# Optimization experiments

Measured on AMD Instinct MI355X. Metric: run time of the kernel, lower is better.

## Reference

```python
import jax, jax.numpy as jnp
import numpy as np


def setup_inputs() -> dict:
    key = jax.random.key(0)
    k1, k2, k3 = jax.random.split(key, 3)
    B, Cin, H, W = 32, 128, 56, 56
    E, Cout = 8, 128
    x = jax.random.normal(k1, (B, Cin, H, W), dtype=jnp.float32)
    conv_w = jax.random.normal(k2, (E, Cout, Cin, 3, 3), dtype=jnp.float32) * 0.05
    gate_w = jax.random.normal(k3, (E, Cin), dtype=jnp.float32) * 0.05
    gate_b = jnp.zeros((E,), dtype=jnp.float32)
    return {"x": x, "conv_w": conv_w, "gate_w": gate_w, "gate_b": gate_b, "top_k": 2}


def reference(x, conv_w, gate_w, gate_b, top_k):
    # x: [B, Cin, H, W]; conv_w: [E, Cout, Cin, 3, 3]
    E, Cout, Cin, kh, kw = conv_w.shape
    B = x.shape[0]
    # Gate: global average pool -> linear logits over experts
    gap = x.mean(axis=(2, 3))                      # [B, Cin]
    logits = gap @ gate_w.T + gate_b               # [B, E]
    vals, idx = jax.lax.top_k(logits, top_k)       # [B, k]
    w = jax.nn.softmax(vals, axis=-1)              # renormalize over selected experts
    weights = jnp.zeros((B, E), dtype=x.dtype).at[jnp.arange(B)[:, None], idx].set(w)
    # All experts via a single conv with stacked output channels (stride=1, pad=1 == SAME)
    y = jax.lax.conv_general_dilated(
        x, conv_w.reshape(E * Cout, Cin, kh, kw),
        window_strides=(1, 1), padding='SAME',
        dimension_numbers=('NCHW', 'OIHW', 'NCHW'))  # [B, E*Cout, H, W]
    y = y.reshape(B, E, Cout, y.shape[2], y.shape[3])
    out = jnp.einsum('be,bechw->bchw', weights, y)  # sparse-weight combine
    return out, weights
```

## Files before the change

### kernel.cpp

```cpp
#include <hip/hip_runtime.h>
#include <hip/hip_bf16.h>

constexpr int Bn   = 32;
constexpr int CIN  = 128;
constexpr int Hh   = 56;
constexpr int Ww   = 56;
constexpr int HW   = Hh * Ww;
constexpr int COUT = 128;
constexpr int En   = 8;

typedef __attribute__((ext_vector_type(8))) short bf16x8;
typedef __attribute__((ext_vector_type(4))) float f32x4;

struct GateInfo { int e0, e1; float w0, w1; };

constexpr size_t XB_OFF  = 0;
constexpr size_t XB_SZ   = (size_t)Bn * HW * CIN * 2;
constexpr size_t WW_OFF  = XB_OFF + XB_SZ;
constexpr size_t WW_SZ   = (size_t)Bn * 9 * COUT * CIN * 2;
constexpr size_t HS_OFF  = WW_OFF + WW_SZ;
constexpr size_t HS_SZ   = (size_t)Bn * Hh * CIN * 4;
constexpr size_t GAP_OFF = HS_OFF + HS_SZ;
constexpr size_t GAP_SZ  = (size_t)Bn * CIN * 4;
constexpr size_t GI_OFF  = GAP_OFF + GAP_SZ;

__global__ __launch_bounds__(256) void convert_kernel(const float* __restrict__ x,
        __hip_bfloat16* __restrict__ xbf, float* __restrict__ hsum) {
    __shared__ float lt[CIN * 57];
    int gid = blockIdx.x;
    int b = gid / Hh, h = gid % Hh;
    const float* xp = x + (size_t)b * CIN * HW + h * Ww;
    for (int u = threadIdx.x; u < CIN * Ww; u += 256) {
        int c = u / Ww, w = u % Ww;
        lt[c * 57 + w] = xp[(size_t)c * HW + w];
    }
    __syncthreads();
    __hip_bfloat16* xo = xbf + ((size_t)b * HW + h * Ww) * CIN;
    for (int u = threadIdx.x; u < CIN * Ww; u += 256) {
        int w = u >> 7, c = u & 127;
        xo[u] = __float2bfloat16(lt[c * 57 + w]);
    }
    if (threadIdx.x < CIN) {
        int c = threadIdx.x;
        float s = 0.f;
        #pragma unroll 8
        for (int w = 0; w < Ww; w++) s += lt[c * 57 + w];
        hsum[((size_t)b * Hh + h) * CIN + c] = s;
    }
}

__global__ void gap2_kernel(const float* __restrict__ hsum, float* __restrict__ gap) {
    int t = blockIdx.x * 256 + threadIdx.x;
    int b = t >> 7, c = t & 127;
    float s = 0.f;
    for (int h = 0; h < Hh; h++) s += hsum[((size_t)b * Hh + h) * CIN + c];
    gap[t] = s * (1.f / (float)HW);
}

__global__ void gate_kernel(const float* __restrict__ gap,
                            const float* __restrict__ gate_w,
                            const float* __restrict__ gate_b,
                            float* __restrict__ wout,
                            GateInfo* __restrict__ info) {
    __shared__ float logits[Bn][En];
    __shared__ GateInfo gi[Bn];
    int tid = threadIdx.x;
    int b = tid >> 3, e = tid & 7;
    float s = gate_b[e];
    const float* g = gap + b * CIN;
    const float* w = gate_w + e * CIN;
    #pragma unroll 8
    for (int c = 0; c < CIN; c++) s += g[c] * w[c];
    logits[b][e] = s;
    __syncthreads();
    if (tid < Bn) {
        float v[En];
        #pragma unroll
        for (int k = 0; k < En; k++) v[k] = logits[tid][k];
        int i0 = 0; float m0 = v[0];
        #pragma unroll
        for (int k = 1; k < En; k++) if (v[k] > m0) { m0 = v[k]; i0 = k; }
        int i1 = -1; float m1 = -1e30f;
        #pragma unroll
        for (int k = 0; k < En; k++) if (k != i0 && v[k] > m1) { m1 = v[k]; i1 = k; }
        float ex = expf(m1 - m0);
        float den = 1.f + ex;
        GateInfo t; t.e0 = i0; t.e1 = i1; t.w0 = 1.f / den; t.w1 = ex / den;
        gi[tid] = t;
        info[tid] = t;
    }
    __syncthreads();
    {
        int bb = tid >> 3, ee = tid & 7;
        GateInfo t = gi[bb];
        wout[tid] = (ee == t.e0) ? t.w0 : (ee == t.e1) ? t.w1 : 0.f;
    }
}

__global__ __launch_bounds__(256) void wcomb_kernel(const float* __restrict__ cw,
        const GateInfo* __restrict__ info, __hip_bfloat16* __restrict__ wws) {
    __shared__ __hip_bfloat16 wl[16 * 1152];
    int b = blockIdx.x >> 3, cg = blockIdx.x & 7;
    GateInfo gi = info[b];
    const float* p0 = cw + (size_t)gi.e0 * COUT * CIN * 9 + (size_t)cg * 16 * 1152;
    const float* p1 = cw + (size_t)gi.e1 * COUT * CIN * 9 + (size_t)cg * 16 * 1152;
    for (int u = threadIdx.x; u < 16 * 1152; u += 256)
        wl[u] = __float2bfloat16(gi.w0 * p0[u] + gi.w1 * p1[u]);
    __syncthreads();
    __hip_bfloat16* wo = wws + (size_t)b * 9 * COUT * CIN + (size_t)cg * 16 * CIN;
    for (int u = threadIdx.x; u < 16 * 1152; u += 256) {
        int t = u / 2048, rem = u & 2047;
        int co = rem >> 7, cin = rem & 127;
        wo[(size_t)t * COUT * CIN + co * CIN + cin] = wl[co * 1152 + cin * 9 + t];
    }
}

constexpr int US = 349;

__global__ __launch_bounds__(256, 2) void conv_mfma(
        const __hip_bfloat16* __restrict__ xbf,
        const __hip_bfloat16* __restrict__ wws,
        float* __restrict__ out) {
    __shared__ char xs[4 * US * 16];

    int gid = blockIdx.x;
    int b = gid / 28, rem = gid % 28;
    int cb = rem / 14, rb = rem % 14;
    int row0 = rb * 4, cout0 = cb * 64;
    int tid = threadIdx.x, wave = tid >> 6, lane = tid & 63;
    int wm = wave >> 1, wn = wave & 1;
    int l15 = lane & 15, lk = lane >> 4;

    int bbase[7];
    #pragma unroll
    for (int i = 0; i < 7; i++) {
        int p = wn * 112 + i * 16 + l15;
        int r = p / 56, c = p % 56;
        bbase[i] = (lk * US + (r * 58 + c)) * 16;
    }

    const __hip_bfloat16* wwb = wws + (size_t)b * 9 * COUT * CIN;
    int arow = cout0 + wm * 32 + l15;

    f32x4 acc[2][7];
    #pragma unroll
    for (int mt = 0; mt < 2; mt++)
        #pragma unroll
        for (int i = 0; i < 7; i++) acc[mt][i] = (f32x4){0.f, 0.f, 0.f, 0.f};

    for (int c0 = 0; c0 < CIN; c0 += 32) {
        __syncthreads();
        const __hip_bfloat16* xbb = xbf + (size_t)b * HW * CIN + c0;
        for (int u = tid; u < 1392; u += 256) {
            int rc = u >> 2, ul = u & 3;
            int lr = rc / 58, lc = rc % 58;
            int grow = row0 - 1 + lr, gw = lc - 1;
            int4 v = {0, 0, 0, 0};
            if ((unsigned)grow < 56u && (unsigned)gw < 56u)
                v = *(const int4*)(xbb + ((size_t)grow * 56 + gw) * CIN + ul * 8);
            *(int4*)(xs + (ul * US + rc) * 16) = v;
        }
        __syncthreads();

        const __hip_bfloat16* ap = wwb + (size_t)arow * CIN + c0 + lk * 8;
        #pragma unroll
        for (int t = 0; t < 9; t++) {
            const int dr = t / 3, dc = t % 3;
            bf16x8 a0 = *(const bf16x8*)(ap + (size_t)t * COUT * CIN);
            bf16x8 a1 = *(const bf16x8*)(ap + (size_t)t * COUT * CIN + 16 * CIN);
            const int toff = (dr * 58 + dc) * 16;
            #pragma unroll
            for (int i = 0; i < 7; i++) {
                bf16x8 bv = *(const bf16x8*)(xs + bbase[i] + toff);
                acc[0][i] = __builtin_amdgcn_mfma_f32_16x16x32_bf16(a0, bv, acc[0][i], 0, 0, 0);
                acc[1][i] = __builtin_amdgcn_mfma_f32_16x16x32_bf16(a1, bv, acc[1][i], 0, 0, 0);
            }
        }
    }

    float* outb = out + (size_t)b * COUT * HW + row0 * 56;
    #pragma unroll
    for (int mt = 0; mt < 2; mt++) {
        int cbase = cout0 + wm * 32 + mt * 16 + lk * 4;
        #pragma unroll
        for (int i = 0; i < 7; i++) {
            int pp = wn * 112 + i * 16 + l15;
            #pragma unroll
            for (int j = 0; j < 4; j++)
                outb[(size_t)(cbase + j) * HW + pp] = acc[mt][i][j];
        }
    }
}

extern "C" void kernel_launch(void* const* d_in, const int* in_sizes, int n_in,
                              void* d_out, int out_size, void* d_ws, size_t ws_size,
                              hipStream_t stream) {
    const float* x  = (const float*)d_in[0];
    const float* cw = (const float*)d_in[1];
    const float* gw = (const float*)d_in[2];
    const float* gb = (const float*)d_in[3];

    float* out = (float*)d_out;
    char* ws = (char*)d_ws;
    __hip_bfloat16* xbf  = (__hip_bfloat16*)(ws + XB_OFF);
    __hip_bfloat16* wws  = (__hip_bfloat16*)(ws + WW_OFF);
    float* hsum          = (float*)(ws + HS_OFF);
    float* gap           = (float*)(ws + GAP_OFF);
    GateInfo* info       = (GateInfo*)(ws + GI_OFF);
    float* wout = out + (size_t)Bn * COUT * HW;

    convert_kernel<<<Bn * Hh, 256, 0, stream>>>(x, xbf, hsum);
    gap2_kernel   <<<16,      256, 0, stream>>>(hsum, gap);
    gate_kernel   <<<1,       256, 0, stream>>>(gap, gw, gb, wout, info);
    wcomb_kernel  <<<Bn * 8,  256, 0, stream>>>(cw, info, wws);
    conv_mfma     <<<Bn * 2 * 14, 256, 0, stream>>>(xbf, wws, out);
}
```

Measured before the change: 182.0 us.

## Enlarge conv tile to 8 rows, map batches to XCDs, vectorize bf16 convert stores

The conv kernel now computes 8 output rows by 64 output channels per block. Each wave owns 112 pixels and all 64 channels, holding 4x7 accumulators, so every B-operand LDS read feeds four MFMAs instead of two. The grid drops to 448 blocks, and block indices are remapped so that blocks of the same batch land on the same XCD, which should improve L2 reuse of activations and weights. The convert kernel now packs 8 bf16 values into one 16-byte store instead of writing scalar bf16. The costs are higher register pressure (launch bounds now ask for 3 blocks per CU), a larger LDS tile, and fewer blocks, so the grid may fill the GPU less well.

After: 188.6 us. +3.6%, slower.

```diff
diff --git a/kernel.cpp b/kernel.cpp
--- a/kernel.cpp
+++ b/kernel.cpp
@@ -36,9 +36,15 @@
     }
     __syncthreads();
     __hip_bfloat16* xo = xbf + ((size_t)b * HW + h * Ww) * CIN;
-    for (int u = threadIdx.x; u < CIN * Ww; u += 256) {
-        int w = u >> 7, c = u & 127;
-        xo[u] = __float2bfloat16(lt[c * 57 + w]);
+    for (int u = threadIdx.x; u < 16 * Ww; u += 256) {
+        int w = u >> 4, cg = u & 15;
+        bf16x8 pk;
+        #pragma unroll
+        for (int j = 0; j < 8; j++) {
+            __hip_bfloat16 t = __float2bfloat16(lt[(cg * 8 + j) * 57 + w]);
+            pk[j] = *reinterpret_cast<short*>(&t);
+        }
+        *(bf16x8*)(xo + (size_t)w * CIN + cg * 8) = pk;
     }
     if (threadIdx.x < CIN) {
         int c = threadIdx.x;
@@ -115,20 +121,22 @@
     }
 }
 
-constexpr int US = 349;
-
-__global__ __launch_bounds__(256, 2) void conv_mfma(
+constexpr int USz = 581;
+
+__global__ __launch_bounds__(256, 3) void conv_mfma(
         const __hip_bfloat16* __restrict__ xbf,
         const __hip_bfloat16* __restrict__ wws,
         float* __restrict__ out) {
-    __shared__ char xs[4 * US * 16];
-
-    int gid = blockIdx.x;
-    int b = gid / 28, rem = gid % 28;
-    int cb = rem / 14, rb = rem % 14;
-    int row0 = rb * 4, cout0 = cb * 64;
+    __shared__ char xs[4 * USz * 16];
+
+    int bid = blockIdx.x;
+    int xcd = bid & 7, k = bid >> 3;
+    int b   = xcd * 4 + k / 14;
+    int rem = k % 14;
+    int cb  = rem / 7, rb = rem % 7;
+    int row0 = rb * 8, cout0 = cb * 64;
     int tid = threadIdx.x, wave = tid >> 6, lane = tid & 63;
-    int wm = wave >> 1, wn = wave & 1;
+    int wn = wave;
     int l15 = lane & 15, lk = lane >> 4;
 
     int bbase[7];
@@ -136,52 +144,55 @@
     for (int i = 0; i < 7; i++) {
         int p = wn * 112 + i * 16 + l15;
         int r = p / 56, c = p % 56;
-        bbase[i] = (lk * US + (r * 58 + c)) * 16;
+        bbase[i] = (lk * USz + (r * 58 + c)) * 16;
     }
 
     const __hip_bfloat16* wwb = wws + (size_t)b * 9 * COUT * CIN;
-    int arow = cout0 + wm * 32 + l15;
-
-    f32x4 acc[2][7];
+    const __hip_bfloat16* ap  = wwb + (size_t)(cout0 + l15) * CIN + lk * 8;
+
+    f32x4 acc[4][7];
     #pragma unroll
-    for (int mt = 0; mt < 2; mt++)
+    for (int mt = 0; mt < 4; mt++)
         #pragma unroll
         for (int i = 0; i < 7; i++) acc[mt][i] = (f32x4){0.f, 0.f, 0.f, 0.f};
 
     for (int c0 = 0; c0 < CIN; c0 += 32) {
         __syncthreads();
         const __hip_bfloat16* xbb = xbf + (size_t)b * HW * CIN + c0;
-        for (int u = tid; u < 1392; u += 256) {
-            int rc = u >> 2, ul = u & 3;
+        for (int u = tid; u < 2320; u += 256) {
+            int ul = u / 580, rc = u % 580;
             int lr = rc / 58, lc = rc % 58;
             int grow = row0 - 1 + lr, gw = lc - 1;
             int4 v = {0, 0, 0, 0};
             if ((unsigned)grow < 56u && (unsigned)gw < 56u)
                 v = *(const int4*)(xbb + ((size_t)grow * 56 + gw) * CIN + ul * 8);
-            *(int4*)(xs + (ul * US + rc) * 16) = v;
+            *(int4*)(xs + (ul * USz + rc) * 16) = v;
         }
         __syncthreads();
 
-        const __hip_bfloat16* ap = wwb + (size_t)arow * CIN + c0 + lk * 8;
         #pragma unroll
         for (int t = 0; t < 9; t++) {
             const int dr = t / 3, dc = t % 3;
-            bf16x8 a0 = *(const bf16x8*)(ap + (size_t)t * COUT * CIN);
-            bf16x8 a1 = *(const bf16x8*)(ap + (size_t)t * COUT * CIN + 16 * CIN);
+            const __hip_bfloat16* at = ap + (size_t)t * COUT * CIN + c0;
+            bf16x8 a[4];
+            #pragma unroll
+            for (int mt = 0; mt < 4; mt++)
+                a[mt] = *(const bf16x8*)(at + mt * 16 * CIN);
             const int toff = (dr * 58 + dc) * 16;
             #pragma unroll
             for (int i = 0; i < 7; i++) {
                 bf16x8 bv = *(const bf16x8*)(xs + bbase[i] + toff);
-                acc[0][i] = __builtin_amdgcn_mfma_f32_16x16x32_bf16(a0, bv, acc[0][i], 0, 0, 0);
-                acc[1][i] = __builtin_amdgcn_mfma_f32_16x16x32_bf16(a1, bv, acc[1][i], 0, 0, 0);
+                #pragma unroll
+                for (int mt = 0; mt < 4; mt++)
+                    acc[mt][i] = __builtin_amdgcn_mfma_f32_16x16x32_bf16(a[mt], bv, acc[mt][i], 0, 0, 0);
             }
         }
     }
 
     float* outb = out + (size_t)b * COUT * HW + row0 * 56;
     #pragma unroll
-    for (int mt = 0; mt < 2; mt++) {
-        int cbase = cout0 + wm * 32 + mt * 16 + lk * 4;
+    for (int mt = 0; mt < 4; mt++) {
+        int cbase = cout0 + mt * 16 + lk * 4;
         #pragma unroll
         for (int i = 0; i < 7; i++) {
             int pp = wn * 112 + i * 16 + l15;
@@ -213,5 +224,5 @@
     gap2_kernel   <<<16,      256, 0, stream>>>(hsum, gap);
     gate_kernel   <<<1,       256, 0, stream>>>(gap, gw, gb, wout, info);
     wcomb_kernel  <<<Bn * 8,  256, 0, stream>>>(cw, info, wws);
-    conv_mfma     <<<Bn * 2 * 14, 256, 0, stream>>>(xbf, wws, out);
-}
+    conv_mfma     <<<448, 256, 0, stream>>>(xbf, wws, out);
+}
```

## Pre-pad input into channel-group planes and double-buffer conv tiles via direct global-to-LDS loads

Applied to the files above, without the earlier changes.

Input is written in a zero-padded layout split into 32-channel planes, so each conv block can copy a contiguous 22 KB slab straight into LDS with global_load_lds. That removes the bounds checks and register staging from the conv loop. The next channel group's slab is loaded into a second LDS buffer while MFMAs run on the current one, which halves the barriers per iteration. The change also remaps block IDs so all blocks of one batch land on the same XCD, raises occupancy to 3 blocks per CU, and vectorises the packing stores in convert and wcomb. In exchange there is an extra zero-padding kernel and twice the LDS per block.

Result: faster. 178.4 us (-2.0%).

```diff
diff --git a/kernel.cpp b/kernel.cpp
--- a/kernel.cpp
+++ b/kernel.cpp
@@ -14,9 +14,12 @@
 
 struct GateInfo { int e0, e1; float w0, w1; };
 
-constexpr size_t XB_OFF  = 0;
-constexpr size_t XB_SZ   = (size_t)Bn * HW * CIN * 2;
-constexpr size_t WW_OFF  = XB_OFF + XB_SZ;
+constexpr size_t ROWB = 58 * 32 * 2;
+constexpr size_t PGB  = 58 * ROWB;
+
+constexpr size_t XP_OFF  = 0;
+constexpr size_t XP_SZ   = (size_t)Bn * 4 * PGB;
+constexpr size_t WW_OFF  = XP_OFF + XP_SZ;
 constexpr size_t WW_SZ   = (size_t)Bn * 9 * COUT * CIN * 2;
 constexpr size_t HS_OFF  = WW_OFF + WW_SZ;
 constexpr size_t HS_SZ   = (size_t)Bn * Hh * CIN * 4;
@@ -24,8 +27,29 @@
 constexpr size_t GAP_SZ  = (size_t)Bn * CIN * 4;
 constexpr size_t GI_OFF  = GAP_OFF + GAP_SZ;
 
+__device__ inline void gload_lds16(const void* g, void* l) {
+    __builtin_amdgcn_global_load_lds(
+        (const __attribute__((address_space(1))) unsigned int*)g,
+        (__attribute__((address_space(3))) unsigned int*)l, 16, 0, 0);
+}
+
+__global__ __launch_bounds__(256) void zero_kernel(char* __restrict__ xpad) {
+    char* pl = xpad + (size_t)blockIdx.x * PGB;
+    for (int u = threadIdx.x; u < 912; u += 256) {
+        size_t off;
+        if (u < 232)      off = (size_t)u * 16;
+        else if (u < 464) off = 57 * ROWB + (size_t)(u - 232) * 16;
+        else {
+            int v = u - 464;
+            int r = v / 8 + 1, s = (v & 7) >> 2, a = v & 3;
+            off = (size_t)r * ROWB + (s ? 57 : 0) * 64 + a * 16;
+        }
+        *(int4*)(pl + off) = (int4){0, 0, 0, 0};
+    }
+}
+
 __global__ __launch_bounds__(256) void convert_kernel(const float* __restrict__ x,
-        __hip_bfloat16* __restrict__ xbf, float* __restrict__ hsum) {
+        char* __restrict__ xpad, float* __restrict__ hsum) {
     __shared__ float lt[CIN * 57];
     int gid = blockIdx.x;
     int b = gid / Hh, h = gid % Hh;
@@ -35,10 +59,16 @@
         lt[c * 57 + w] = xp[(size_t)c * HW + w];
     }
     __syncthreads();
-    __hip_bfloat16* xo = xbf + ((size_t)b * HW + h * Ww) * CIN;
-    for (int u = threadIdx.x; u < CIN * Ww; u += 256) {
-        int w = u >> 7, c = u & 127;
-        xo[u] = __float2bfloat16(lt[c * 57 + w]);
+    char* dst = xpad + (size_t)b * 4 * PGB + (size_t)(h + 1) * ROWB;
+    for (int u = threadIdx.x; u < 896; u += 256) {
+        int g = u / 224, r = u % 224, w = r >> 2, a = r & 3;
+        bf16x8 pk;
+        #pragma unroll
+        for (int j = 0; j < 8; j++) {
+            __hip_bfloat16 t = __float2bfloat16(lt[(g * 32 + a * 8 + j) * 57 + w]);
+            pk[j] = *reinterpret_cast<short*>(&t);
+        }
+        *(bf16x8*)(dst + (size_t)g * PGB + (size_t)(w + 1) * 64 + a * 16) = pk;
     }
     if (threadIdx.x < CIN) {
         int c = threadIdx.x;
@@ -108,39 +138,43 @@
         wl[u] = __float2bfloat16(gi.w0 * p0[u] + gi.w1 * p1[u]);
     __syncthreads();
     __hip_bfloat16* wo = wws + (size_t)b * 9 * COUT * CIN + (size_t)cg * 16 * CIN;
-    for (int u = threadIdx.x; u < 16 * 1152; u += 256) {
-        int t = u / 2048, rem = u & 2047;
-        int co = rem >> 7, cin = rem & 127;
-        wo[(size_t)t * COUT * CIN + co * CIN + cin] = wl[co * 1152 + cin * 9 + t];
-    }
-}
-
-constexpr int US = 349;
-
-__global__ __launch_bounds__(256, 2) void conv_mfma(
-        const __hip_bfloat16* __restrict__ xbf,
+    for (int u = threadIdx.x; u < 2304; u += 256) {
+        int t = u >> 8, rem = u & 255, co = rem >> 4, a = rem & 15;
+        bf16x8 pk;
+        #pragma unroll
+        for (int j = 0; j < 8; j++)
+            pk[j] = *reinterpret_cast<short*>(&wl[co * 1152 + (a * 8 + j) * 9 + t]);
+        *(bf16x8*)(wo + (size_t)t * COUT * CIN + co * CIN + a * 8) = pk;
+    }
+}
+
+__global__ __launch_bounds__(256, 3) void conv_mfma(
+        const char* __restrict__ xpad,
         const __hip_bfloat16* __restrict__ wws,
         float* __restrict__ out) {
-    __shared__ char xs[4 * US * 16];
-
-    int gid = blockIdx.x;
-    int b = gid / 28, rem = gid % 28;
-    int cb = rem / 14, rb = rem % 14;
+    __shared__ char xs[2][22528];
+
+    int bid = blockIdx.x;
+    int xcd = bid & 7, k = bid >> 3;
+    int b   = xcd * 4 + k / 28;
+    int r2  = k % 28;
+    int cb  = r2 / 14, rb = r2 % 14;
     int row0 = rb * 4, cout0 = cb * 64;
     int tid = threadIdx.x, wave = tid >> 6, lane = tid & 63;
     int wm = wave >> 1, wn = wave & 1;
     int l15 = lane & 15, lk = lane >> 4;
 
+    const char* src = xpad + (size_t)b * 4 * PGB + (size_t)row0 * ROWB;
+
     int bbase[7];
     #pragma unroll
     for (int i = 0; i < 7; i++) {
         int p = wn * 112 + i * 16 + l15;
-        int r = p / 56, c = p % 56;
-        bbase[i] = (lk * US + (r * 58 + c)) * 16;
-    }
-
-    const __hip_bfloat16* wwb = wws + (size_t)b * 9 * COUT * CIN;
-    int arow = cout0 + wm * 32 + l15;
+        bbase[i] = (p / 56) * (int)ROWB + (p % 56) * 64 + lk * 16;
+    }
+
+    const __hip_bfloat16* ap = wws + (size_t)b * 9 * COUT * CIN
+                             + (size_t)(cout0 + wm * 32 + l15) * CIN + lk * 8;
 
     f32x4 acc[2][7];
     #pragma unroll
@@ -148,30 +182,36 @@
         #pragma unroll
         for (int i = 0; i < 7; i++) acc[mt][i] = (f32x4){0.f, 0.f, 0.f, 0.f};
 
-    for (int c0 = 0; c0 < CIN; c0 += 32) {
+    #pragma unroll
+    for (int i2 = 0; i2 < 6; i2++) {
+        int idx = i2 * 4 + wave;
+        if (idx < 22)
+            gload_lds16(src + idx * 1024 + lane * 16, &xs[0][idx * 1024]);
+    }
+
+    for (int g = 0; g < 4; ++g) {
         __syncthreads();
-        const __hip_bfloat16* xbb = xbf + (size_t)b * HW * CIN + c0;
-        for (int u = tid; u < 1392; u += 256) {
-            int rc = u >> 2, ul = u & 3;
-            int lr = rc / 58, lc = rc % 58;
-            int grow = row0 - 1 + lr, gw = lc - 1;
-            int4 v = {0, 0, 0, 0};
-            if ((unsigned)grow < 56u && (unsigned)gw < 56u)
-                v = *(const int4*)(xbb + ((size_t)grow * 56 + gw) * CIN + ul * 8);
-            *(int4*)(xs + (ul * US + rc) * 16) = v;
-        }
-        __syncthreads();
-
-        const __hip_bfloat16* ap = wwb + (size_t)arow * CIN + c0 + lk * 8;
+        if (g < 3) {
+            const char* s2 = src + (size_t)(g + 1) * PGB;
+            #pragma unroll
+            for (int i2 = 0; i2 < 6; i2++) {
+                int idx = i2 * 4 + wave;
+                if (idx < 22)
+                    gload_lds16(s2 + idx * 1024 + lane * 16, &xs[(g + 1) & 1][idx * 1024]);
+            }
+        }
+        const char* xb = xs[g & 1];
+        const __hip_bfloat16* at0 = ap + g * 32;
         #pragma unroll
         for (int t = 0; t < 9; t++) {
             const int dr = t / 3, dc = t % 3;
-            bf16x8 a0 = *(const bf16x8*)(ap + (size_t)t * COUT * CIN);
-            bf16x8 a1 = *(const bf16x8*)(ap + (size_t)t * COUT * CIN + 16 * CIN);
-            const int toff = (dr * 58 + dc) * 16;
+            const __hip_bfloat16* at = at0 + (size_t)t * COUT * CIN;
+            bf16x8 a0 = *(const bf16x8*)(at);
+            bf16x8 a1 = *(const bf16x8*)(at + 16 * CIN);
+            const int toff = dr * (int)ROWB + dc * 64;
             #pragma unroll
             for (int i = 0; i < 7; i++) {
-                bf16x8 bv = *(const bf16x8*)(xs + bbase[i] + toff);
+                bf16x8 bv = *(const bf16x8*)(xb + bbase[i] + toff);
                 acc[0][i] = __builtin_amdgcn_mfma_f32_16x16x32_bf16(a0, bv, acc[0][i], 0, 0, 0);
                 acc[1][i] = __builtin_amdgcn_mfma_f32_16x16x32_bf16(a1, bv, acc[1][i], 0, 0, 0);
             }
@@ -202,16 +242,17 @@
 
     float* out = (float*)d_out;
     char* ws = (char*)d_ws;
-    __hip_bfloat16* xbf  = (__hip_bfloat16*)(ws + XB_OFF);
+    char* xpad           = ws + XP_OFF;
     __hip_bfloat16* wws  = (__hip_bfloat16*)(ws + WW_OFF);
     float* hsum          = (float*)(ws + HS_OFF);
     float* gap           = (float*)(ws + GAP_OFF);
     GateInfo* info       = (GateInfo*)(ws + GI_OFF);
     float* wout = out + (size_t)Bn * COUT * HW;
 
-    convert_kernel<<<Bn * Hh, 256, 0, stream>>>(x, xbf, hsum);
+    zero_kernel   <<<Bn * 4,  256, 0, stream>>>(xpad);
+    convert_kernel<<<Bn * Hh, 256, 0, stream>>>(x, xpad, hsum);
     gap2_kernel   <<<16,      256, 0, stream>>>(hsum, gap);
     gate_kernel   <<<1,       256, 0, stream>>>(gap, gw, gb, wout, info);
     wcomb_kernel  <<<Bn * 8,  256, 0, stream>>>(cw, info, wws);
-    conv_mfma     <<<Bn * 2 * 14, 256, 0, stream>>>(xbf, wws, out);
-}
+    conv_mfma     <<<896,     256, 0, stream>>>(xpad, wws, out);
+}
```
